# Kernel tuning notes

Hardware: AMD Instinct MI355X
Metric: run time of the kernel (lower is better)

Reference implementation:

```python
import jax, jax.numpy as jnp
import numpy as np

N_NODES = 100000
N_EDGES = 1600000
IN_CH, HID_CH, OUT_CH = 128, 128, 64


def _sage_conv(x, src, dst, Wl, bl, Wr, num_nodes):
    # PyG SAGEConv (aggr='mean', root_weight=True):
    #   out_i = W_l @ mean_{j in N(i)} x_j + b_l + W_r @ x_i
    msgs = x[src]                                            # [E, d] gather
    agg = jax.ops.segment_sum(msgs, dst, num_segments=num_nodes)   # [N, d]
    cnt = jax.ops.segment_sum(jnp.ones((src.shape[0],), x.dtype), dst,
                              num_segments=num_nodes)              # [N]
    mean = agg / jnp.maximum(cnt, 1.0)[:, None]
    return mean @ Wl.T + bl + x @ Wr.T


def setup_inputs() -> dict:
    key = jax.random.key(0)
    ks = jax.random.split(key, 8)
    x = jax.random.normal(ks[0], (N_NODES, IN_CH), dtype=jnp.float32)
    edge_index = jax.random.randint(ks[1], (2, N_EDGES), 0, N_NODES, dtype=jnp.int32)
    s1 = 1.0 / np.sqrt(IN_CH)
    s2 = 1.0 / np.sqrt(HID_CH)
    Wl1 = jax.random.uniform(ks[2], (HID_CH, IN_CH), jnp.float32, -s1, s1)
    bl1 = jax.random.uniform(ks[3], (HID_CH,), jnp.float32, -s1, s1)
    Wr1 = jax.random.uniform(ks[4], (HID_CH, IN_CH), jnp.float32, -s1, s1)
    Wl2 = jax.random.uniform(ks[5], (OUT_CH, HID_CH), jnp.float32, -s2, s2)
    bl2 = jax.random.uniform(ks[6], (OUT_CH,), jnp.float32, -s2, s2)
    Wr2 = jax.random.uniform(ks[7], (OUT_CH, HID_CH), jnp.float32, -s2, s2)
    return {"x": x, "edge_index": edge_index, "Wl1": Wl1, "bl1": bl1,
            "Wr1": Wr1, "Wl2": Wl2, "bl2": bl2, "Wr2": Wr2}


def reference(x, edge_index, Wl1, bl1, Wr1, Wl2, bl2, Wr2):
    src, dst = edge_index[0], edge_index[1]
    n = x.shape[0]
    h = _sage_conv(x, src, dst, Wl1, bl1, Wr1, n)
    h = jax.nn.relu(h)  # dropout is identity in eval mode
    out = _sage_conv(h, src, dst, Wl2, bl2, Wr2, n)
    return out
```

## Files before the change

kernel.cpp:

```cpp
#include <hip/hip_runtime.h>
#include <hip/hip_bf16.h>
#include <stdint.h>

#define IN_CH 128
#define NPB   448
#define NBUCK 224
#define CAP   8192
#define PART_EPB 2048
#define SRC_BITS 17
#define SRC_MASK ((1 << SRC_BITS) - 1)

typedef short v8s __attribute__((ext_vector_type(8)));
typedef float v4f __attribute__((ext_vector_type(4)));
typedef float v2f __attribute__((ext_vector_type(2)));
typedef ushort v4u __attribute__((ext_vector_type(4)));

__device__ __forceinline__ ushort f2b(float f) {
    return ((__hip_bfloat16_raw)__float2bfloat16(f)).x;
}
__device__ __forceinline__ float b2f(ushort u) {
    __hip_bfloat16_raw r; r.x = u;
    return __bfloat162float((__hip_bfloat16)r);
}

#define ACC4(r) {                                                            \
    a01 += (v2f){__uint_as_float((r).x << 16),                               \
                 __uint_as_float((r).x & 0xffff0000u)};                      \
    a23 += (v2f){__uint_as_float((r).y << 16),                               \
                 __uint_as_float((r).y & 0xffff0000u)};                      \
    a45 += (v2f){__uint_as_float((r).z << 16),                               \
                 __uint_as_float((r).z & 0xffff0000u)};                      \
    a67 += (v2f){__uint_as_float((r).w << 16),                               \
                 __uint_as_float((r).w & 0xffff0000u)}; }

__global__ __launch_bounds__(256) void k_part(
    const int* __restrict__ src, const int* __restrict__ dst,
    int* __restrict__ cursor, int* __restrict__ ebuf, int E) {
    __shared__ int sedge[PART_EPB];
    __shared__ int h[NBUCK], lofs[NBUCK], gbase[NBUCK], lcur[NBUCK];
    __shared__ int ssc[256];

    int tid = threadIdx.x;
    int eb0 = blockIdx.x * PART_EPB;
    int cnt = min(PART_EPB, E - eb0);

    if (tid < NBUCK) { h[tid] = 0; lcur[tid] = 0; }
    __syncthreads();
    for (int i = tid; i < cnt; i += 256)
        atomicAdd(&h[dst[eb0 + i] / NPB], 1);
    __syncthreads();
    int v = (tid < NBUCK) ? h[tid] : 0;
    ssc[tid] = v;
    __syncthreads();
    for (int off = 1; off < 256; off <<= 1) {
        int val = (tid >= off) ? ssc[tid - off] : 0;
        __syncthreads();
        ssc[tid] += val;
        __syncthreads();
    }
    int excl = ssc[tid] - v;
    if (tid < NBUCK) {
        lofs[tid] = excl;
        gbase[tid] = tid * CAP + atomicAdd(&cursor[tid], v);
    }
    __syncthreads();
    for (int i = tid; i < cnt; i += 256) {
        int s0 = src[eb0 + i];
        int d0 = dst[eb0 + i];
        int b = d0 / NPB;
        int dl = d0 - b * NPB;
        int p = atomicAdd(&lcur[b], 1);
        sedge[lofs[b] + p] = (dl << SRC_BITS) | s0;
    }
    __syncthreads();
    for (int i = tid; i < cnt; i += 256) {
        int lo = 0, hi = NBUCK - 1;
        while (lo < hi) {
            int mid = (lo + hi + 1) >> 1;
            if (lofs[mid] <= i) lo = mid; else hi = mid - 1;
        }
        int pos = gbase[lo] + (i - lofs[lo]);
        if (pos < (lo + 1) * CAP) ebuf[pos] = sedge[i];
    }
}

__global__ __launch_bounds__(256) void k_bbuild_gemm1(
    const int* __restrict__ ebuf, const int* __restrict__ cursor,
    int2* __restrict__ rowdeg, int* __restrict__ col,
    const float* __restrict__ Af,
    const float* __restrict__ WlF, const float* __restrict__ WrF,
    ushort* __restrict__ qb, ushort* __restrict__ pbb, int N) {
    const int OC = 256;
    const int NT = OC / 16;
    const int LDW = 128 + 8;
    __shared__ ushort Wlds[OC * LDW];
    __shared__ int sdeg[NPB];
    __shared__ int scur[NPB];
    __shared__ int ssum[256];

    int tid = threadIdx.x;

    if (blockIdx.x < NBUCK) {
        int b = blockIdx.x;
        int base = b * NPB;
        int nodes = min(NPB, N - base);
        int e0 = b * CAP;
        int e1 = e0 + min(cursor[b], CAP);

        for (int i = tid; i < NPB; i += 256) sdeg[i] = 0;
        __syncthreads();
        for (int e = e0 + tid; e < e1; e += 256)
            atomicAdd(&sdeg[((unsigned)ebuf[e]) >> SRC_BITS], 1);
        __syncthreads();
        int d0 = 0, d1 = 0;
        if (tid < 224) { d0 = sdeg[2 * tid]; d1 = sdeg[2 * tid + 1]; }
        int ts = d0 + d1;
        ssum[tid] = ts;
        __syncthreads();
        for (int off = 1; off < 256; off <<= 1) {
            int val = (tid >= off) ? ssum[tid - off] : 0;
            __syncthreads();
            ssum[tid] += val;
            __syncthreads();
        }
        int excl = ssum[tid] - ts;
        if (tid < 224) {
            scur[2 * tid] = excl;
            scur[2 * tid + 1] = excl + d0;
            if (2 * tid < nodes)
                rowdeg[base + 2 * tid] = make_int2(e0 + excl, d0);
            if (2 * tid + 1 < nodes)
                rowdeg[base + 2 * tid + 1] = make_int2(e0 + excl + d0, d1);
        }
        __syncthreads();
        for (int e = e0 + tid; e < e1; e += 256) {
            int w = ebuf[e];
            int dl = ((unsigned)w) >> SRC_BITS;
            int p = atomicAdd(&scur[dl], 1);
            col[e0 + p] = w & SRC_MASK;
        }
        return;
    }

    int gb = blockIdx.x - NBUCK;
    if (gb == 0 && tid < 16) {
        v8s z = {0, 0, 0, 0, 0, 0, 0, 0};
        *(v8s*)(qb + (size_t)N * 128 + tid * 8) = z;
    }

    for (int it = 0; it < OC / 16; it++) {
        int idx = it * 256 + tid;
        int r = idx >> 4, kc = (idx & 15) * 8;
        const float* Wrow = (r < OC / 2) ? (WlF + (size_t)r * 128)
                                         : (WrF + (size_t)(r - OC / 2) * 128);
        float4 w0 = *(const float4*)(Wrow + kc);
        float4 w1 = *(const float4*)(Wrow + kc + 4);
        v8s wv;
        wv[0] = (short)f2b(w0.x); wv[1] = (short)f2b(w0.y);
        wv[2] = (short)f2b(w0.z); wv[3] = (short)f2b(w0.w);
        wv[4] = (short)f2b(w1.x); wv[5] = (short)f2b(w1.y);
        wv[6] = (short)f2b(w1.z); wv[7] = (short)f2b(w1.w);
        *(v8s*)((short*)Wlds + r * LDW + kc) = wv;
    }
    __syncthreads();

    int wave = tid >> 6;
    int lane = tid & 63;
    int m16 = lane & 15;
    int quad = lane >> 4;
    int rowbase = gb * 128 + wave * 32;

    v4f acc[2][NT];
#pragma unroll
    for (int mt = 0; mt < 2; mt++)
#pragma unroll
        for (int t = 0; t < NT; t++) acc[mt][t] = {0.f, 0.f, 0.f, 0.f};

    int ar0 = min(rowbase + m16, N - 1);
    int ar1 = min(rowbase + 16 + m16, N - 1);

#pragma unroll
    for (int ks = 0; ks < 4; ks++) {
        int k0 = ks * 32 + quad * 8;
        float4 f00 = *(const float4*)(Af + (size_t)ar0 * 128 + k0);
        float4 f01 = *(const float4*)(Af + (size_t)ar0 * 128 + k0 + 4);
        float4 f10 = *(const float4*)(Af + (size_t)ar1 * 128 + k0);
        float4 f11 = *(const float4*)(Af + (size_t)ar1 * 128 + k0 + 4);
        v8s a0, a1;
        a0[0] = (short)f2b(f00.x); a0[1] = (short)f2b(f00.y);
        a0[2] = (short)f2b(f00.z); a0[3] = (short)f2b(f00.w);
        a0[4] = (short)f2b(f01.x); a0[5] = (short)f2b(f01.y);
        a0[6] = (short)f2b(f01.z); a0[7] = (short)f2b(f01.w);
        a1[0] = (short)f2b(f10.x); a1[1] = (short)f2b(f10.y);
        a1[2] = (short)f2b(f10.z); a1[3] = (short)f2b(f10.w);
        a1[4] = (short)f2b(f11.x); a1[5] = (short)f2b(f11.y);
        a1[6] = (short)f2b(f11.z); a1[7] = (short)f2b(f11.w);
#pragma unroll
        for (int t = 0; t < NT; t++) {
            v8s b = *(const v8s*)((const short*)Wlds + (t * 16 + m16) * LDW + k0);
            acc[0][t] = __builtin_amdgcn_mfma_f32_16x16x32_bf16(a0, b, acc[0][t], 0, 0, 0);
            acc[1][t] = __builtin_amdgcn_mfma_f32_16x16x32_bf16(a1, b, acc[1][t], 0, 0, 0);
        }
    }

#pragma unroll
    for (int mt = 0; mt < 2; mt++) {
        int orow0 = rowbase + mt * 16 + quad * 4;
#pragma unroll
        for (int r = 0; r < 4; r++) {
            int orow = orow0 + r;
            if (orow < N) {
#pragma unroll
                for (int t = 0; t < NT; t++) {
                    int c = t * 16 + m16;
                    float v = acc[mt][t][r];
                    if (c < 128) qb[(size_t)orow * 128 + c] = f2b(v);
                    else pbb[(size_t)orow * 128 + (c - 128)] = f2b(v);
                }
            }
        }
    }
}

__global__ __launch_bounds__(256) void k_wgemm2(
    const ushort* __restrict__ Ab,
    const float* __restrict__ WlF, const float* __restrict__ WrF,
    ushort* __restrict__ qb, float* __restrict__ pbf, int N) {
    const int OC = 128;
    const int NT = OC / 16;
    const int LDW = 128 + 8;
    __shared__ ushort Wlds[OC * LDW];

    int tid = threadIdx.x;
    if (blockIdx.x == 0 && tid < 8) {
        v8s z = {0, 0, 0, 0, 0, 0, 0, 0};
        *(v8s*)(qb + (size_t)N * 64 + tid * 8) = z;
    }
    for (int it = 0; it < OC / 16; it++) {
        int idx = it * 256 + tid;
        int r = idx >> 4, kc = (idx & 15) * 8;
        const float* Wrow = (r < OC / 2) ? (WlF + (size_t)r * 128)
                                         : (WrF + (size_t)(r - OC / 2) * 128);
        float4 w0 = *(const float4*)(Wrow + kc);
        float4 w1 = *(const float4*)(Wrow + kc + 4);
        v8s wv;
        wv[0] = (short)f2b(w0.x); wv[1] = (short)f2b(w0.y);
        wv[2] = (short)f2b(w0.z); wv[3] = (short)f2b(w0.w);
        wv[4] = (short)f2b(w1.x); wv[5] = (short)f2b(w1.y);
        wv[6] = (short)f2b(w1.z); wv[7] = (short)f2b(w1.w);
        *(v8s*)((short*)Wlds + r * LDW + kc) = wv;
    }
    __syncthreads();

    int wave = tid >> 6;
    int lane = tid & 63;
    int m16 = lane & 15;
    int quad = lane >> 4;
    int rowbase = blockIdx.x * 128 + wave * 32;

    v4f acc[2][NT];
#pragma unroll
    for (int mt = 0; mt < 2; mt++)
#pragma unroll
        for (int t = 0; t < NT; t++) acc[mt][t] = {0.f, 0.f, 0.f, 0.f};

    int ar0 = min(rowbase + m16, N - 1);
    int ar1 = min(rowbase + 16 + m16, N - 1);

#pragma unroll
    for (int ks = 0; ks < 4; ks++) {
        int k0 = ks * 32 + quad * 8;
        v8s a0 = *(const v8s*)((const short*)Ab + (size_t)ar0 * 128 + k0);
        v8s a1 = *(const v8s*)((const short*)Ab + (size_t)ar1 * 128 + k0);
#pragma unroll
        for (int t = 0; t < NT; t++) {
            v8s b = *(const v8s*)((const short*)Wlds + (t * 16 + m16) * LDW + k0);
            acc[0][t] = __builtin_amdgcn_mfma_f32_16x16x32_bf16(a0, b, acc[0][t], 0, 0, 0);
            acc[1][t] = __builtin_amdgcn_mfma_f32_16x16x32_bf16(a1, b, acc[1][t], 0, 0, 0);
        }
    }

#pragma unroll
    for (int mt = 0; mt < 2; mt++) {
        int orow0 = rowbase + mt * 16 + quad * 4;
#pragma unroll
        for (int r = 0; r < 4; r++) {
            int orow = orow0 + r;
            if (orow < N) {
#pragma unroll
                for (int t = 0; t < NT; t++) {
                    int c = t * 16 + m16;
                    float v = acc[mt][t][r];
                    if (c < 64) qb[(size_t)orow * 64 + c] = f2b(v);
                    else pbf[(size_t)orow * 64 + (c - 64)] = v;
                }
            }
        }
    }
}

__global__ __launch_bounds__(256, 8) void k_agg1(
    const int2* __restrict__ rowdeg,
    const int* __restrict__ col, const ushort* __restrict__ q1b,
    const ushort* __restrict__ p1b, const float* __restrict__ bias,
    ushort* __restrict__ hb, int N) {
    int node = blockIdx.x * (blockDim.x >> 6) + (threadIdx.x >> 6);
    int lane = threadIdx.x & 63;
    if (node >= N) return;
    int2 rd = rowdeg[node];
    int s0 = rd.x, dn = rd.y;
    int s1 = s0 + dn;
    int g = lane >> 4;
    int ch = 8 * (lane & 15);
    v4u pb = *(const v4u*)((const ushort*)p1b + (size_t)node * 128 + ch);
    v4u pb2 = *(const v4u*)((const ushort*)p1b + (size_t)node * 128 + ch + 4);
    int last = (dn > 0) ? (s1 - 1) : s0;
    v2f a01 = {0.f, 0.f}, a23 = {0.f, 0.f}, a45 = {0.f, 0.f}, a67 = {0.f, 0.f};
    int j = s0;
    do {
        int i0 = j + g,      i1 = j + 4 + g,  i2 = j + 8 + g,  i3 = j + 12 + g;
        int i4 = j + 16 + g, i5 = j + 20 + g, i6 = j + 24 + g, i7 = j + 28 + g;
        int t0 = col[min(i0, last)];
        int t1 = col[min(i1, last)];
        int t2 = col[min(i2, last)];
        int t3 = col[min(i3, last)];
        int t4 = col[min(i4, last)];
        int t5 = col[min(i5, last)];
        int t6 = col[min(i6, last)];
        int t7 = col[min(i7, last)];
        int c0 = (i0 < s1) ? t0 : N;
        int c1 = (i1 < s1) ? t1 : N;
        int c2 = (i2 < s1) ? t2 : N;
        int c3 = (i3 < s1) ? t3 : N;
        int c4 = (i4 < s1) ? t4 : N;
        int c5 = (i5 < s1) ? t5 : N;
        int c6 = (i6 < s1) ? t6 : N;
        int c7 = (i7 < s1) ? t7 : N;
        uint4 r0 = *(const uint4*)(q1b + (size_t)c0 * 128 + ch);
        uint4 r1 = *(const uint4*)(q1b + (size_t)c1 * 128 + ch);
        uint4 r2 = *(const uint4*)(q1b + (size_t)c2 * 128 + ch);
        uint4 r3 = *(const uint4*)(q1b + (size_t)c3 * 128 + ch);
        uint4 r4 = *(const uint4*)(q1b + (size_t)c4 * 128 + ch);
        uint4 r5 = *(const uint4*)(q1b + (size_t)c5 * 128 + ch);
        uint4 r6 = *(const uint4*)(q1b + (size_t)c6 * 128 + ch);
        uint4 r7 = *(const uint4*)(q1b + (size_t)c7 * 128 + ch);
        ACC4(r0); ACC4(r1); ACC4(r2); ACC4(r3);
        ACC4(r4); ACC4(r5); ACC4(r6); ACC4(r7);
        j += 32;
    } while (j < s1);
    float s[8] = {a01.x, a01.y, a23.x, a23.y, a45.x, a45.y, a67.x, a67.y};
#pragma unroll
    for (int k = 0; k < 8; k++) {
        s[k] += __shfl_xor(s[k], 16);
        s[k] += __shfl_xor(s[k], 32);
    }
    if (g == 0) {
        float inv = (dn > 0) ? 1.0f / (float)dn : 0.0f;
        float4 bi0 = *(const float4*)(bias + ch);
        float4 bi1 = *(const float4*)(bias + ch + 4);
        v8s o;
        o[0] = (short)f2b(fmaxf(s[0] * inv + b2f(pb.x) + bi0.x, 0.f));
        o[1] = (short)f2b(fmaxf(s[1] * inv + b2f(pb.y) + bi0.y, 0.f));
        o[2] = (short)f2b(fmaxf(s[2] * inv + b2f(pb.z) + bi0.z, 0.f));
        o[3] = (short)f2b(fmaxf(s[3] * inv + b2f(pb.w) + bi0.w, 0.f));
        o[4] = (short)f2b(fmaxf(s[4] * inv + b2f(pb2.x) + bi1.x, 0.f));
        o[5] = (short)f2b(fmaxf(s[5] * inv + b2f(pb2.y) + bi1.y, 0.f));
        o[6] = (short)f2b(fmaxf(s[6] * inv + b2f(pb2.z) + bi1.z, 0.f));
        o[7] = (short)f2b(fmaxf(s[7] * inv + b2f(pb2.w) + bi1.w, 0.f));
        *(v8s*)(hb + (size_t)node * 128 + ch) = o;
    }
}

__global__ __launch_bounds__(256, 8) void k_agg2(
    const int2* __restrict__ rowdeg,
    const int* __restrict__ col, const ushort* __restrict__ q2,
    const float* __restrict__ p2, const float* __restrict__ bias,
    float* __restrict__ out, int N) {
    int node = blockIdx.x * (blockDim.x >> 6) + (threadIdx.x >> 6);
    int lane = threadIdx.x & 63;
    if (node >= N) return;
    int2 rd = rowdeg[node];
    int s0 = rd.x, dn = rd.y;
    int s1 = s0 + dn;
    int g = lane >> 3;
    int ch = 8 * (lane & 7);
    v4f p0 = *(const v4f*)(p2 + (size_t)node * 64 + ch);
    v4f p1 = *(const v4f*)(p2 + (size_t)node * 64 + ch + 4);
    int last = (dn > 0) ? (s1 - 1) : s0;
    v2f a01 = {0.f, 0.f}, a23 = {0.f, 0.f}, a45 = {0.f, 0.f}, a67 = {0.f, 0.f};
    int j = s0;
    do {
        int i0 = j + g, i1 = j + 8 + g, i2 = j + 16 + g, i3 = j + 24 + g;
        int t0 = col[min(i0, last)];
        int t1 = col[min(i1, last)];
        int t2 = col[min(i2, last)];
        int t3 = col[min(i3, last)];
        int c0 = (i0 < s1) ? t0 : N;
        int c1 = (i1 < s1) ? t1 : N;
        int c2 = (i2 < s1) ? t2 : N;
        int c3 = (i3 < s1) ? t3 : N;
        uint4 r0 = *(const uint4*)(q2 + (size_t)c0 * 64 + ch);
        uint4 r1 = *(const uint4*)(q2 + (size_t)c1 * 64 + ch);
        uint4 r2 = *(const uint4*)(q2 + (size_t)c2 * 64 + ch);
        uint4 r3 = *(const uint4*)(q2 + (size_t)c3 * 64 + ch);
        ACC4(r0); ACC4(r1); ACC4(r2); ACC4(r3);
        j += 32;
    } while (j < s1);
    float s[8] = {a01.x, a01.y, a23.x, a23.y, a45.x, a45.y, a67.x, a67.y};
#pragma unroll
    for (int k = 0; k < 8; k++) {
        s[k] += __shfl_xor(s[k], 8);
        s[k] += __shfl_xor(s[k], 16);
        s[k] += __shfl_xor(s[k], 32);
    }
    if (g == 0) {
        float inv = (dn > 0) ? 1.0f / (float)dn : 0.0f;
        float4 bi0 = *(const float4*)(bias + ch);
        float4 bi1 = *(const float4*)(bias + ch + 4);
        v4f o0, o1;
        o0[0] = s[0] * inv + p0[0] + bi0.x;
        o0[1] = s[1] * inv + p0[1] + bi0.y;
        o0[2] = s[2] * inv + p0[2] + bi0.z;
        o0[3] = s[3] * inv + p0[3] + bi0.w;
        o1[0] = s[4] * inv + p1[0] + bi1.x;
        o1[1] = s[5] * inv + p1[1] + bi1.y;
        o1[2] = s[6] * inv + p1[2] + bi1.z;
        o1[3] = s[7] * inv + p1[3] + bi1.w;
        *(v4f*)(out + (size_t)node * 64 + ch) = o0;
        *(v4f*)(out + (size_t)node * 64 + ch + 4) = o1;
    }
}

extern "C" void kernel_launch(void* const* d_in, const int* in_sizes, int n_in,
                              void* d_out, int out_size, void* d_ws, size_t ws_size,
                              hipStream_t stream) {
    const float* x   = (const float*)d_in[0];
    const int* ei    = (const int*)d_in[1];
    const float* Wl1 = (const float*)d_in[2];
    const float* bl1 = (const float*)d_in[3];
    const float* Wr1 = (const float*)d_in[4];
    const float* Wl2 = (const float*)d_in[5];
    const float* bl2 = (const float*)d_in[6];
    const float* Wr2 = (const float*)d_in[7];

    const int N = in_sizes[0] / IN_CH;
    const int E = in_sizes[1] / 2;
    const int* src = ei;
    const int* dst = ei + E;

    char* p = (char*)d_ws;
    auto carve = [&](size_t bytes) -> void* {
        void* q = (void*)p;
        p += (bytes + 255) & ~(size_t)255;
        return q;
    };
    int* cursor   = (int*)carve(NBUCK * 4);
    int* ebuf     = (int*)carve((size_t)NBUCK * CAP * 4);
    int* col      = (int*)carve((size_t)NBUCK * CAP * 4 + 256);
    int2* rowdeg  = (int2*)carve((size_t)N * 8);
    ushort* q1b   = (ushort*)carve(((size_t)N + 1) * 128 * 2);
    ushort* p1b   = (ushort*)carve((size_t)N * 128 * 2);
    ushort* hb    = (ushort*)carve((size_t)N * 128 * 2);
    ushort* q2    = (ushort*)carve(((size_t)N + 1) * 64 * 2);
    float* p2     = (float*)carve((size_t)N * 64 * 4);
    (void)ws_size; (void)n_in;

    float* out = (float*)d_out;
    (void)out_size;

    const int GB1 = (N + 127) / 128;

    (void)hipMemsetAsync(cursor, 0, NBUCK * 4, stream);
    k_part<<<(E + PART_EPB - 1) / PART_EPB, 256, 0, stream>>>(src, dst, cursor, ebuf, E);
    k_bbuild_gemm1<<<NBUCK + GB1, 256, 0, stream>>>(
        ebuf, cursor, rowdeg, col, x, Wl1, Wr1, q1b, p1b, N);

    k_agg1<<<(N + 3) / 4, 256, 0, stream>>>(rowdeg, col, q1b, p1b, bl1, hb, N);

    k_wgemm2<<<GB1, 256, 0, stream>>>(hb, Wl2, Wr2, q2, p2, N);
    k_agg2<<<(N + 3) / 4, 256, 0, stream>>>(rowdeg, col, q2, p2, bl2, out, N);
}
```

Measured before the change: 282.3 us.

## Fuse edge partitioning with first GEMM and split bucket build into own kernel

Moves the independent layer-1 GEMM blocks into the partition kernel launch so the GEMM work overlaps with edge bucketing, and moves the CSR bucket build into its own kernel. The partition step now caches dst in shared memory and stores a per-slot bucket id, which removes the second dst read and the per-edge binary search. Gather address math in both aggregation kernels switches from 64-bit to 32-bit, which cuts integer instructions. The cost is one extra kernel launch. The merged kernel uses a large shared-memory block, which may lower occupancy for the partition blocks.

```diff
diff --git a/kernel.cpp b/kernel.cpp
--- a/kernel.cpp
+++ b/kernel.cpp
@@ -33,116 +33,76 @@
     a67 += (v2f){__uint_as_float((r).w << 16),                               \
                  __uint_as_float((r).w & 0xffff0000u)}; }
 
-__global__ __launch_bounds__(256) void k_part(
+__global__ __launch_bounds__(256) void k_part_gemm1(
     const int* __restrict__ src, const int* __restrict__ dst,
-    int* __restrict__ cursor, int* __restrict__ ebuf, int E) {
-    __shared__ int sedge[PART_EPB];
-    __shared__ int h[NBUCK], lofs[NBUCK], gbase[NBUCK], lcur[NBUCK];
-    __shared__ int ssc[256];
-
-    int tid = threadIdx.x;
-    int eb0 = blockIdx.x * PART_EPB;
-    int cnt = min(PART_EPB, E - eb0);
-
-    if (tid < NBUCK) { h[tid] = 0; lcur[tid] = 0; }
-    __syncthreads();
-    for (int i = tid; i < cnt; i += 256)
-        atomicAdd(&h[dst[eb0 + i] / NPB], 1);
-    __syncthreads();
-    int v = (tid < NBUCK) ? h[tid] : 0;
-    ssc[tid] = v;
-    __syncthreads();
-    for (int off = 1; off < 256; off <<= 1) {
-        int val = (tid >= off) ? ssc[tid - off] : 0;
-        __syncthreads();
-        ssc[tid] += val;
-        __syncthreads();
-    }
-    int excl = ssc[tid] - v;
-    if (tid < NBUCK) {
-        lofs[tid] = excl;
-        gbase[tid] = tid * CAP + atomicAdd(&cursor[tid], v);
-    }
-    __syncthreads();
-    for (int i = tid; i < cnt; i += 256) {
-        int s0 = src[eb0 + i];
-        int d0 = dst[eb0 + i];
-        int b = d0 / NPB;
-        int dl = d0 - b * NPB;
-        int p = atomicAdd(&lcur[b], 1);
-        sedge[lofs[b] + p] = (dl << SRC_BITS) | s0;
-    }
-    __syncthreads();
-    for (int i = tid; i < cnt; i += 256) {
-        int lo = 0, hi = NBUCK - 1;
-        while (lo < hi) {
-            int mid = (lo + hi + 1) >> 1;
-            if (lofs[mid] <= i) lo = mid; else hi = mid - 1;
-        }
-        int pos = gbase[lo] + (i - lofs[lo]);
-        if (pos < (lo + 1) * CAP) ebuf[pos] = sedge[i];
-    }
-}
-
-__global__ __launch_bounds__(256) void k_bbuild_gemm1(
-    const int* __restrict__ ebuf, const int* __restrict__ cursor,
-    int2* __restrict__ rowdeg, int* __restrict__ col,
+    int* __restrict__ cursor, int* __restrict__ ebuf, int E, int PB,
     const float* __restrict__ Af,
     const float* __restrict__ WlF, const float* __restrict__ WrF,
     ushort* __restrict__ qb, ushort* __restrict__ pbb, int N) {
+    __shared__ __align__(16) char smem[69632];
+    int tid = threadIdx.x;
+
+    if ((int)blockIdx.x < PB) {
+        int* sedge = (int*)smem;
+        int* sdst  = (int*)(smem + 8192);
+        int* h     = (int*)(smem + 16384);
+        int* lofs  = h + NBUCK;
+        int* gbase = lofs + NBUCK;
+        int* lcur  = gbase + NBUCK;
+        int* ssc   = lcur + NBUCK;
+        unsigned char* sbuck = (unsigned char*)(ssc + 256);
+
+        int eb0 = blockIdx.x * PART_EPB;
+        int cnt = min(PART_EPB, E - eb0);
+
+        if (tid < NBUCK) { h[tid] = 0; lcur[tid] = 0; }
+        __syncthreads();
+        for (int i = tid; i < cnt; i += 256) {
+            int d = dst[eb0 + i];
+            sdst[i] = d;
+            atomicAdd(&h[d / NPB], 1);
+        }
+        __syncthreads();
+        int v = (tid < NBUCK) ? h[tid] : 0;
+        ssc[tid] = v;
+        __syncthreads();
+        for (int off = 1; off < 256; off <<= 1) {
+            int val = (tid >= off) ? ssc[tid - off] : 0;
+            __syncthreads();
+            ssc[tid] += val;
+            __syncthreads();
+        }
+        int excl = ssc[tid] - v;
+        if (tid < NBUCK) {
+            lofs[tid] = excl;
+            gbase[tid] = tid * CAP + atomicAdd(&cursor[tid], v);
+        }
+        __syncthreads();
+        for (int i = tid; i < cnt; i += 256) {
+            int s0 = src[eb0 + i];
+            int d0 = sdst[i];
+            int b = d0 / NPB;
+            int dl = d0 - b * NPB;
+            int p = atomicAdd(&lcur[b], 1);
+            int slot = lofs[b] + p;
+            sedge[slot] = (dl << SRC_BITS) | s0;
+            sbuck[slot] = (unsigned char)b;
+        }
+        __syncthreads();
+        for (int i = tid; i < cnt; i += 256) {
+            int b = sbuck[i];
+            int pos = gbase[b] + (i - lofs[b]);
+            if (pos < (b + 1) * CAP) ebuf[pos] = sedge[i];
+        }
+        return;
+    }
+
     const int OC = 256;
     const int NT = OC / 16;
     const int LDW = 128 + 8;
-    __shared__ ushort Wlds[OC * LDW];
-    __shared__ int sdeg[NPB];
-    __shared__ int scur[NPB];
-    __shared__ int ssum[256];
-
-    int tid = threadIdx.x;
-
-    if (blockIdx.x < NBUCK) {
-        int b = blockIdx.x;
-        int base = b * NPB;
-        int nodes = min(NPB, N - base);
-        int e0 = b * CAP;
-        int e1 = e0 + min(cursor[b], CAP);
-
-        for (int i = tid; i < NPB; i += 256) sdeg[i] = 0;
-        __syncthreads();
-        for (int e = e0 + tid; e < e1; e += 256)
-            atomicAdd(&sdeg[((unsigned)ebuf[e]) >> SRC_BITS], 1);
-        __syncthreads();
-        int d0 = 0, d1 = 0;
-        if (tid < 224) { d0 = sdeg[2 * tid]; d1 = sdeg[2 * tid + 1]; }
-        int ts = d0 + d1;
-        ssum[tid] = ts;
-        __syncthreads();
-        for (int off = 1; off < 256; off <<= 1) {
-            int val = (tid >= off) ? ssum[tid - off] : 0;
-            __syncthreads();
-            ssum[tid] += val;
-            __syncthreads();
-        }
-        int excl = ssum[tid] - ts;
-        if (tid < 224) {
-            scur[2 * tid] = excl;
-            scur[2 * tid + 1] = excl + d0;
-            if (2 * tid < nodes)
-                rowdeg[base + 2 * tid] = make_int2(e0 + excl, d0);
-            if (2 * tid + 1 < nodes)
-                rowdeg[base + 2 * tid + 1] = make_int2(e0 + excl + d0, d1);
-        }
-        __syncthreads();
-        for (int e = e0 + tid; e < e1; e += 256) {
-            int w = ebuf[e];
-            int dl = ((unsigned)w) >> SRC_BITS;
-            int p = atomicAdd(&scur[dl], 1);
-            col[e0 + p] = w & SRC_MASK;
-        }
-        return;
-    }
-
-    int gb = blockIdx.x - NBUCK;
+    ushort* Wlds = (ushort*)smem;
+
+    int gb = blockIdx.x - PB;
     if (gb == 0 && tid < 16) {
         v8s z = {0, 0, 0, 0, 0, 0, 0, 0};
         *(v8s*)(qb + (size_t)N * 128 + tid * 8) = z;
@@ -219,6 +179,52 @@
                 }
             }
         }
+    }
+}
+
+__global__ __launch_bounds__(256) void k_bbuild(
+    const int* __restrict__ ebuf, const int* __restrict__ cursor,
+    int2* __restrict__ rowdeg, int* __restrict__ col, int N) {
+    __shared__ int sdeg[NPB];
+    __shared__ int scur[NPB];
+    __shared__ int ssum[256];
+    int b = blockIdx.x, tid = threadIdx.x;
+    int base = b * NPB;
+    int nodes = min(NPB, N - base);
+    int e0 = b * CAP;
+    int e1 = e0 + min(cursor[b], CAP);
+
+    for (int i = tid; i < NPB; i += 256) sdeg[i] = 0;
+    __syncthreads();
+    for (int e = e0 + tid; e < e1; e += 256)
+        atomicAdd(&sdeg[((unsigned)ebuf[e]) >> SRC_BITS], 1);
+    __syncthreads();
+    int d0 = 0, d1 = 0;
+    if (tid < 224) { d0 = sdeg[2 * tid]; d1 = sdeg[2 * tid + 1]; }
+    int ts = d0 + d1;
+    ssum[tid] = ts;
+    __syncthreads();
+    for (int off = 1; off < 256; off <<= 1) {
+        int val = (tid >= off) ? ssum[tid - off] : 0;
+        __syncthreads();
+        ssum[tid] += val;
+        __syncthreads();
+    }
+    int excl = ssum[tid] - ts;
+    if (tid < 224) {
+        scur[2 * tid] = excl;
+        scur[2 * tid + 1] = excl + d0;
+        if (2 * tid < nodes)
+            rowdeg[base + 2 * tid] = make_int2(e0 + excl, d0);
+        if (2 * tid + 1 < nodes)
+            rowdeg[base + 2 * tid + 1] = make_int2(e0 + excl + d0, d1);
+    }
+    __syncthreads();
+    for (int e = e0 + tid; e < e1; e += 256) {
+        int w = ebuf[e];
+        int dl = ((unsigned)w) >> SRC_BITS;
+        int p = atomicAdd(&scur[dl], 1);
+        col[e0 + p] = w & SRC_MASK;
     }
 }
 
@@ -336,14 +342,14 @@
         int c5 = (i5 < s1) ? t5 : N;
         int c6 = (i6 < s1) ? t6 : N;
         int c7 = (i7 < s1) ? t7 : N;
-        uint4 r0 = *(const uint4*)(q1b + (size_t)c0 * 128 + ch);
-        uint4 r1 = *(const uint4*)(q1b + (size_t)c1 * 128 + ch);
-        uint4 r2 = *(const uint4*)(q1b + (size_t)c2 * 128 + ch);
-        uint4 r3 = *(const uint4*)(q1b + (size_t)c3 * 128 + ch);
-        uint4 r4 = *(const uint4*)(q1b + (size_t)c4 * 128 + ch);
-        uint4 r5 = *(const uint4*)(q1b + (size_t)c5 * 128 + ch);
-        uint4 r6 = *(const uint4*)(q1b + (size_t)c6 * 128 + ch);
-        uint4 r7 = *(const uint4*)(q1b + (size_t)c7 * 128 + ch);
+        uint4 r0 = *(const uint4*)(q1b + ((uint)c0 * 128u + (uint)ch));
+        uint4 r1 = *(const uint4*)(q1b + ((uint)c1 * 128u + (uint)ch));
+        uint4 r2 = *(const uint4*)(q1b + ((uint)c2 * 128u + (uint)ch));
+        uint4 r3 = *(const uint4*)(q1b + ((uint)c3 * 128u + (uint)ch));
+        uint4 r4 = *(const uint4*)(q1b + ((uint)c4 * 128u + (uint)ch));
+        uint4 r5 = *(const uint4*)(q1b + ((uint)c5 * 128u + (uint)ch));
+        uint4 r6 = *(const uint4*)(q1b + ((uint)c6 * 128u + (uint)ch));
+        uint4 r7 = *(const uint4*)(q1b + ((uint)c7 * 128u + (uint)ch));
         ACC4(r0); ACC4(r1); ACC4(r2); ACC4(r3);
         ACC4(r4); ACC4(r5); ACC4(r6); ACC4(r7);
         j += 32;
@@ -399,10 +405,10 @@
         int c1 = (i1 < s1) ? t1 : N;
         int c2 = (i2 < s1) ? t2 : N;
         int c3 = (i3 < s1) ? t3 : N;
-        uint4 r0 = *(const uint4*)(q2 + (size_t)c0 * 64 + ch);
-        uint4 r1 = *(const uint4*)(q2 + (size_t)c1 * 64 + ch);
-        uint4 r2 = *(const uint4*)(q2 + (size_t)c2 * 64 + ch);
-        uint4 r3 = *(const uint4*)(q2 + (size_t)c3 * 64 + ch);
+        uint4 r0 = *(const uint4*)(q2 + ((uint)c0 * 64u + (uint)ch));
+        uint4 r1 = *(const uint4*)(q2 + ((uint)c1 * 64u + (uint)ch));
+        uint4 r2 = *(const uint4*)(q2 + ((uint)c2 * 64u + (uint)ch));
+        uint4 r3 = *(const uint4*)(q2 + ((uint)c3 * 64u + (uint)ch));
         ACC4(r0); ACC4(r1); ACC4(r2); ACC4(r3);
         j += 32;
     } while (j < s1);
@@ -468,15 +474,17 @@
     float* out = (float*)d_out;
     (void)out_size;
 
-    const int GB1 = (N + 127) / 128;
+    const int PB  = (E + PART_EPB - 1) / PART_EPB;
+    const int GB  = (N + 127) / 128;
 
     (void)hipMemsetAsync(cursor, 0, NBUCK * 4, stream);
-    k_part<<<(E + PART_EPB - 1) / PART_EPB, 256, 0, stream>>>(src, dst, cursor, ebuf, E);
-    k_bbuild_gemm1<<<NBUCK + GB1, 256, 0, stream>>>(
-        ebuf, cursor, rowdeg, col, x, Wl1, Wr1, q1b, p1b, N);
+    k_part_gemm1<<<PB + GB, 256, 0, stream>>>(
+        src, dst, cursor, ebuf, E, PB, x, Wl1, Wr1, q1b, p1b, N);
+
+    k_bbuild<<<NBUCK, 256, 0, stream>>>(ebuf, cursor, rowdeg, col, N);
 
     k_agg1<<<(N + 3) / 4, 256, 0, stream>>>(rowdeg, col, q1b, p1b, bl1, hb, N);
 
-    k_wgemm2<<<GB1, 256, 0, stream>>>(hb, Wl2, Wr2, q2, p2, N);
+    k_wgemm2<<<GB, 256, 0, stream>>>(hb, Wl2, Wr2, q2, p2, N);
     k_agg2<<<(N + 3) / 4, 256, 0, stream>>>(rowdeg, col, q2, p2, bl2, out, N);
 }
```

Result: no change. 284.3 us (+0.7%).
